# Kernel optimization log

Measured on AMD Instinct MI355X. Metric: run time of the kernel, lower is better.

Reference implementation:

```python
import jax, jax.numpy as jnp
import numpy as np

N_HEADS = 16
D_EMBED = 1024
D_HEAD = D_EMBED // N_HEADS  # 64
B, S = 2, 2048


def setup_inputs() -> dict:
    key = jax.random.key(0)
    ks = jax.random.split(key, 6)
    k = jax.random.normal(ks[0], (B, S, D_EMBED), dtype=jnp.float32)
    q = jax.random.normal(ks[1], (B, S, D_EMBED), dtype=jnp.float32)
    v = jax.random.normal(ks[2], (B, S, D_EMBED), dtype=jnp.float32)
    # per-head projections, shared across heads (nn.Linear(d_head, d_head, bias=False))
    scale = 1.0 / np.sqrt(D_HEAD)
    Wk = jax.random.normal(ks[3], (D_HEAD, D_HEAD), dtype=jnp.float32) * scale
    Wq = jax.random.normal(ks[4], (D_HEAD, D_HEAD), dtype=jnp.float32) * scale
    Wv = jax.random.normal(ks[5], (D_HEAD, D_HEAD), dtype=jnp.float32) * scale
    return {"k": k, "q": q, "v": v, "Wk": Wk, "Wq": Wq, "Wv": Wv}


def reference(k, q, v, Wk, Wq, Wv):
    b, s, _ = k.shape
    # split heads: [b, s, h, dh]
    kh = k.reshape(b, s, N_HEADS, D_HEAD)
    qh = q.reshape(b, s, N_HEADS, D_HEAD)
    vh = v.reshape(b, s, N_HEADS, D_HEAD)
    # shared per-head linear projection (y = x @ W^T, torch Linear convention)
    kh = jnp.einsum('bshd,ed->bshe', kh, Wk)
    qh = jnp.einsum('bshd,ed->bshe', qh, Wq)
    vh = jnp.einsum('bshd,ed->bshe', vh, Wv)
    # attention scores [b, h, q, k]
    scores = jnp.einsum('bqhd,bkhd->bhqk', qh, kh) / np.sqrt(D_HEAD).astype(np.float32)
    attn = jax.nn.softmax(scores, axis=-1)
    out = jnp.einsum('bhqk,bkhd->bqhd', attn, vh)
    return out.reshape(b, s, D_EMBED)
```

## Files before the change

### kernel.cpp

```cpp
#include <hip/hip_runtime.h>
#include <hip/hip_bf16.h>

typedef unsigned short u16;
typedef __bf16 bf16x8 __attribute__((ext_vector_type(8)));
typedef float f32x4 __attribute__((ext_vector_type(4)));

#define S_LEN 2048
#define NH 16
#define NB 2
#define HEAD_ELEMS (NB * NH * S_LEN * 64)

#if __has_builtin(__builtin_amdgcn_exp2f)
#define EXP2(x) __builtin_amdgcn_exp2f(x)
#else
#define EXP2(x) exp2f(x)
#endif

#define QSCALE 0.180336880f
#define SHIFT2 30.0f

__device__ __forceinline__ bf16x8 pack8(float4 a, float4 b, float sc) {
    union { bf16x8 v; __hip_bfloat162 h[4]; } r;
    r.h[0] = __float22bfloat162_rn(make_float2(a.x * sc, a.y * sc));
    r.h[1] = __float22bfloat162_rn(make_float2(a.z * sc, a.w * sc));
    r.h[2] = __float22bfloat162_rn(make_float2(b.x * sc, b.y * sc));
    r.h[3] = __float22bfloat162_rn(make_float2(b.z * sc, b.w * sc));
    return r.v;
}

__global__ __launch_bounds__(256) void proj_mfma(
    const float* __restrict__ kin, const float* __restrict__ qin, const float* __restrict__ vin,
    const float* __restrict__ Wk, const float* __restrict__ Wq, const float* __restrict__ Wv,
    u16* __restrict__ Kh, u16* __restrict__ Qh, u16* __restrict__ Vt)
{
    const int tid = threadIdx.x;
    const int wave = tid >> 6;
    const int lane = tid & 63;
    const int quad = lane >> 4;
    const int l15 = lane & 15;
    const int wid = blockIdx.x * 4 + wave;
    const int stile = wid >> 3;
    const int hg = wid & 7;
    const long row0 = (long)stile * 16;
    const int b = (int)(row0 >> 11);
    const int s0 = (int)(row0 & 2047);

    bf16x8 wf[3][4][2];
    const float* Ws[3] = {Wk, Wq, Wv};
    #pragma unroll
    for (int p = 0; p < 3; ++p) {
        const float sc = (p == 1) ? QSCALE : 1.0f;
        #pragma unroll
        for (int t = 0; t < 4; ++t) {
            const float* wr = Ws[p] + (t * 16 + l15) * 64 + quad * 8;
            wf[p][t][0] = pack8(*(const float4*)(wr),      *(const float4*)(wr + 4),  sc);
            wf[p][t][1] = pack8(*(const float4*)(wr + 32), *(const float4*)(wr + 36), sc);
        }
    }

    const float* xs[3] = {kin, qin, vin};

    #pragma unroll
    for (int hp = 0; hp < 2; ++hp) {
        const int h = hg * 2 + hp;
        const int bh = b * NH + h;
        bf16x8 xf[3][2];
        #pragma unroll
        for (int p = 0; p < 3; ++p) {
            const float* xr = xs[p] + (row0 + l15) * 1024 + h * 64 + quad * 8;
            xf[p][0] = pack8(*(const float4*)(xr),      *(const float4*)(xr + 4),  1.0f);
            xf[p][1] = pack8(*(const float4*)(xr + 32), *(const float4*)(xr + 36), 1.0f);
        }

        #pragma unroll
        for (int p = 0; p < 2; ++p) {
            u16* dst = (p == 0 ? Kh : Qh) + (long)bh * S_LEN * 64;
            #pragma unroll
            for (int nt = 0; nt < 4; ++nt) {
                f32x4 c = (f32x4){0.f, 0.f, 0.f, 0.f};
                c = __builtin_amdgcn_mfma_f32_16x16x32_bf16(xf[p][0], wf[p][nt][0], c, 0, 0, 0);
                c = __builtin_amdgcn_mfma_f32_16x16x32_bf16(xf[p][1], wf[p][nt][1], c, 0, 0, 0);
                #pragma unroll
                for (int r = 0; r < 4; ++r) {
                    union { __hip_bfloat162 h; u16 u[2]; } t2;
                    t2.h = __float22bfloat162_rn(make_float2(c[r], 0.f));
                    dst[((long)(s0 + quad * 4 + r)) * 64 + nt * 16 + l15] = t2.u[0];
                }
            }
        }

        {
            u16* dst = Vt + (long)bh * 64 * S_LEN;
            #pragma unroll
            for (int dt = 0; dt < 4; ++dt) {
                f32x4 c = (f32x4){0.f, 0.f, 0.f, 0.f};
                c = __builtin_amdgcn_mfma_f32_16x16x32_bf16(wf[2][dt][0], xf[2][0], c, 0, 0, 0);
                c = __builtin_amdgcn_mfma_f32_16x16x32_bf16(wf[2][dt][1], xf[2][1], c, 0, 0, 0);
                #pragma unroll
                for (int r = 0; r < 4; ++r) {
                    union { __hip_bfloat162 h; u16 u[2]; } t2;
                    t2.h = __float22bfloat162_rn(make_float2(c[r], 0.f));
                    dst[((long)(dt * 16 + quad * 4 + r)) * S_LEN + s0 + l15] = t2.u[0];
                }
            }
        }
    }
}

__global__ __launch_bounds__(256, 2) void attn_kernel(
    const u16* __restrict__ Qh, const u16* __restrict__ Kh,
    const u16* __restrict__ Vt, float* __restrict__ out)
{
    __shared__ __align__(16) u16 Pld[4][16 * 72];
    __shared__ __align__(16) float Old[4][64 * 40];
    __shared__ float lbc[4][64];

    const int tid = threadIdx.x;
    const int wave = tid >> 6;
    const int lane = tid & 63;
    const int quad = lane >> 4;
    const int l15 = lane & 15;
    const int qb = blockIdx.x;
    const int bh = blockIdx.y;
    const int b = bh >> 4, h = bh & 15;
    const int q0 = qb * 64;
    const u16* kb = Kh + (long)bh * S_LEN * 64;
    const u16* vb = Vt + (long)bh * 64 * S_LEN;

    bf16x8 qf[4][2];
    {
        const u16* qp = Qh + (long)bh * S_LEN * 64;
        #pragma unroll
        for (int g = 0; g < 4; ++g) {
            const u16* qr = qp + (long)(q0 + g * 16 + l15) * 64 + quad * 8;
            qf[g][0] = *(const bf16x8*)(qr);
            qf[g][1] = *(const bf16x8*)(qr + 32);
        }
    }

    const int rot = 16 * (l15 & 3);
    u16* pbase = &Pld[wave][l15 * 72];
    const int pwc[4] = {( 0 + quad * 4 + rot) & 63, (16 + quad * 4 + rot) & 63,
                        (32 + quad * 4 + rot) & 63, (48 + quad * 4 + rot) & 63};
    const int prc[2] = {(quad * 8 + rot) & 63, (32 + quad * 8 + rot) & 63};

    f32x4 oacc[4][4];
    #pragma unroll
    for (int g = 0; g < 4; ++g)
        #pragma unroll
        for (int dt = 0; dt < 4; ++dt) oacc[g][dt] = (f32x4){0.f, 0.f, 0.f, 0.f};
    float rs[4] = {0.f, 0.f, 0.f, 0.f};

    for (int kt = wave; kt < S_LEN / 64; kt += 4) {
        const u16* kt_p = kb + (long)kt * 64 * 64;
        const u16* vt_p = vb + kt * 64;
        bf16x8 kf[4][2], vf[4][2];
        #pragma unroll
        for (int n = 0; n < 4; ++n) {
            const u16* kr = kt_p + (n * 16 + l15) * 64 + quad * 8;
            kf[n][0] = *(const bf16x8*)(kr);
            kf[n][1] = *(const bf16x8*)(kr + 32);
        }
        #pragma unroll
        for (int dt = 0; dt < 4; ++dt) {
            const u16* vr = vt_p + (long)(dt * 16 + l15) * S_LEN + quad * 8;
            vf[dt][0] = *(const bf16x8*)(vr);
            vf[dt][1] = *(const bf16x8*)(vr + 32);
        }

        #pragma unroll
        for (int g = 0; g < 4; ++g) {
            f32x4 sacc[4];
            #pragma unroll
            for (int n = 0; n < 4; ++n) {
                f32x4 c = (f32x4){0.f, 0.f, 0.f, 0.f};
                c = __builtin_amdgcn_mfma_f32_16x16x32_bf16(kf[n][0], qf[g][0], c, 0, 0, 0);
                c = __builtin_amdgcn_mfma_f32_16x16x32_bf16(kf[n][1], qf[g][1], c, 0, 0, 0);
                sacc[n] = c;
            }
            #pragma unroll
            for (int n = 0; n < 4; ++n) {
                float p0 = EXP2(sacc[n][0] - SHIFT2);
                float p1 = EXP2(sacc[n][1] - SHIFT2);
                float p2 = EXP2(sacc[n][2] - SHIFT2);
                float p3 = EXP2(sacc[n][3] - SHIFT2);
                rs[g] += (p0 + p1) + (p2 + p3);
                union { uint2 w; __hip_bfloat162 h[2]; } pk;
                pk.h[0] = __float22bfloat162_rn(make_float2(p0, p1));
                pk.h[1] = __float22bfloat162_rn(make_float2(p2, p3));
                *(uint2*)(pbase + pwc[n]) = pk.w;
            }
            bf16x8 pf0 = *(const bf16x8*)(pbase + prc[0]);
            bf16x8 pf1 = *(const bf16x8*)(pbase + prc[1]);
            #pragma unroll
            for (int dt = 0; dt < 4; ++dt) {
                f32x4 o = oacc[g][dt];
                o = __builtin_amdgcn_mfma_f32_16x16x32_bf16(vf[dt][0], pf0, o, 0, 0, 0);
                o = __builtin_amdgcn_mfma_f32_16x16x32_bf16(vf[dt][1], pf1, o, 0, 0, 0);
                oacc[g][dt] = o;
            }
        }
    }

    #pragma unroll
    for (int g = 0; g < 4; ++g) {
        rs[g] += __shfl_xor(rs[g], 16);
        rs[g] += __shfl_xor(rs[g], 32);
    }
    if (lane < 16) {
        #pragma unroll
        for (int g = 0; g < 4; ++g) lbc[wave][g * 16 + lane] = rs[g];
    }

    const int rq = tid >> 2, seg = tid & 3;
    #pragma unroll
    for (int half = 0; half < 2; ++half) {
        #pragma unroll
        for (int g = 0; g < 4; ++g)
            #pragma unroll
            for (int d2 = 0; d2 < 2; ++d2)
                *(f32x4*)&Old[wave][(g * 16 + l15) * 40 + d2 * 16 + quad * 4] = oacc[g][half * 2 + d2];
        __syncthreads();
        f32x4 a0 = (f32x4){0.f, 0.f, 0.f, 0.f}, a1 = a0;
        #pragma unroll
        for (int w = 0; w < 4; ++w) {
            a0 += *(const f32x4*)&Old[w][rq * 40 + seg * 8];
            a1 += *(const f32x4*)&Old[w][rq * 40 + seg * 8 + 4];
        }
        const float linv = 1.0f / (lbc[0][rq] + lbc[1][rq] + lbc[2][rq] + lbc[3][rq]);
        float* op = out + ((long)(b * S_LEN + q0 + rq)) * 1024 + h * 64 + half * 32 + seg * 8;
        float4 s0 = make_float4(a0[0] * linv, a0[1] * linv, a0[2] * linv, a0[3] * linv);
        float4 s1 = make_float4(a1[0] * linv, a1[1] * linv, a1[2] * linv, a1[3] * linv);
        *(float4*)(op) = s0;
        *(float4*)(op + 4) = s1;
        __syncthreads();
    }
}

extern "C" void kernel_launch(void* const* d_in, const int* in_sizes, int n_in,
                              void* d_out, int out_size, void* d_ws, size_t ws_size,
                              hipStream_t stream) {
    const float* kin = (const float*)d_in[0];
    const float* qin = (const float*)d_in[1];
    const float* vin = (const float*)d_in[2];
    const float* Wk  = (const float*)d_in[3];
    const float* Wq  = (const float*)d_in[4];
    const float* Wv  = (const float*)d_in[5];
    float* out = (float*)d_out;

    u16* wsp = (u16*)d_ws;
    u16* Kh = wsp;
    u16* Qh = wsp + (long)HEAD_ELEMS;
    u16* Vt = wsp + 2 * (long)HEAD_ELEMS;

    proj_mfma<<<512, 256, 0, stream>>>(kin, qin, vin, Wk, Wq, Wv, Kh, Qh, Vt);
    dim3 g(S_LEN / 64, NB * NH);
    attn_kernel<<<g, 256, 0, stream>>>(Qh, Kh, Vt, out);
}
```

Measured before the change: 177.7 us.

## Split projection into K/Q and V kernels with LDS-staged coalesced stores; prefetch K in attention

Splits the combined projection kernel into separate K/Q and V kernels. Each stages its bf16 results in shared memory and then writes them to global memory with 16-byte coalesced stores, replacing the scattered 2-byte stores. The attention kernel now prefetches the next K tile into registers, uses launch_bounds occupancy 3, and shrinks the output reduction buffer to four phases of 16 columns. This adds one more kernel launch and extra register pressure from the prefetch buffers.

After: 374.7 us. +110.9%, slower.

```diff
diff --git a/kernel.cpp b/kernel.cpp
--- a/kernel.cpp
+++ b/kernel.cpp
@@ -28,91 +28,131 @@
     return r.v;
 }
 
-__global__ __launch_bounds__(256) void proj_mfma(
-    const float* __restrict__ kin, const float* __restrict__ qin, const float* __restrict__ vin,
-    const float* __restrict__ Wk, const float* __restrict__ Wq, const float* __restrict__ Wv,
-    u16* __restrict__ Kh, u16* __restrict__ Qh, u16* __restrict__ Vt)
+__global__ __launch_bounds__(256) void proj_kq(
+    const float* __restrict__ kin, const float* __restrict__ qin,
+    const float* __restrict__ Wk, const float* __restrict__ Wq,
+    u16* __restrict__ Kh, u16* __restrict__ Qh)
 {
+    __shared__ __align__(16) u16 Yld[8 * 16 * 72];
+
     const int tid = threadIdx.x;
     const int wave = tid >> 6;
     const int lane = tid & 63;
     const int quad = lane >> 4;
     const int l15 = lane & 15;
-    const int wid = blockIdx.x * 4 + wave;
-    const int stile = wid >> 3;
-    const int hg = wid & 7;
+    const int stile = blockIdx.x;
+    const int p = blockIdx.y;
+    const int hh = blockIdx.z;
     const long row0 = (long)stile * 16;
     const int b = (int)(row0 >> 11);
     const int s0 = (int)(row0 & 2047);
 
-    bf16x8 wf[3][4][2];
-    const float* Ws[3] = {Wk, Wq, Wv};
-    #pragma unroll
-    for (int p = 0; p < 3; ++p) {
-        const float sc = (p == 1) ? QSCALE : 1.0f;
-        #pragma unroll
-        for (int t = 0; t < 4; ++t) {
-            const float* wr = Ws[p] + (t * 16 + l15) * 64 + quad * 8;
-            wf[p][t][0] = pack8(*(const float4*)(wr),      *(const float4*)(wr + 4),  sc);
-            wf[p][t][1] = pack8(*(const float4*)(wr + 32), *(const float4*)(wr + 36), sc);
-        }
-    }
-
-    const float* xs[3] = {kin, qin, vin};
+    const float* X = p ? qin : kin;
+    const float* W = p ? Wq : Wk;
+    const float sc = p ? QSCALE : 1.0f;
+
+    bf16x8 wf[4][2];
+    #pragma unroll
+    for (int nt = 0; nt < 4; ++nt) {
+        const float* wr = W + (nt * 16 + l15) * 64 + quad * 8;
+        wf[nt][0] = pack8(*(const float4*)(wr),      *(const float4*)(wr + 4),  sc);
+        wf[nt][1] = pack8(*(const float4*)(wr + 32), *(const float4*)(wr + 36), sc);
+    }
 
     #pragma unroll
     for (int hp = 0; hp < 2; ++hp) {
-        const int h = hg * 2 + hp;
-        const int bh = b * NH + h;
-        bf16x8 xf[3][2];
-        #pragma unroll
-        for (int p = 0; p < 3; ++p) {
-            const float* xr = xs[p] + (row0 + l15) * 1024 + h * 64 + quad * 8;
-            xf[p][0] = pack8(*(const float4*)(xr),      *(const float4*)(xr + 4),  1.0f);
-            xf[p][1] = pack8(*(const float4*)(xr + 32), *(const float4*)(xr + 36), 1.0f);
-        }
-
-        #pragma unroll
-        for (int p = 0; p < 2; ++p) {
-            u16* dst = (p == 0 ? Kh : Qh) + (long)bh * S_LEN * 64;
-            #pragma unroll
-            for (int nt = 0; nt < 4; ++nt) {
-                f32x4 c = (f32x4){0.f, 0.f, 0.f, 0.f};
-                c = __builtin_amdgcn_mfma_f32_16x16x32_bf16(xf[p][0], wf[p][nt][0], c, 0, 0, 0);
-                c = __builtin_amdgcn_mfma_f32_16x16x32_bf16(xf[p][1], wf[p][nt][1], c, 0, 0, 0);
-                #pragma unroll
-                for (int r = 0; r < 4; ++r) {
-                    union { __hip_bfloat162 h; u16 u[2]; } t2;
-                    t2.h = __float22bfloat162_rn(make_float2(c[r], 0.f));
-                    dst[((long)(s0 + quad * 4 + r)) * 64 + nt * 16 + l15] = t2.u[0];
-                }
-            }
-        }
-
-        {
-            u16* dst = Vt + (long)bh * 64 * S_LEN;
-            #pragma unroll
-            for (int dt = 0; dt < 4; ++dt) {
-                f32x4 c = (f32x4){0.f, 0.f, 0.f, 0.f};
-                c = __builtin_amdgcn_mfma_f32_16x16x32_bf16(wf[2][dt][0], xf[2][0], c, 0, 0, 0);
-                c = __builtin_amdgcn_mfma_f32_16x16x32_bf16(wf[2][dt][1], xf[2][1], c, 0, 0, 0);
-                #pragma unroll
-                for (int r = 0; r < 4; ++r) {
-                    union { __hip_bfloat162 h; u16 u[2]; } t2;
-                    t2.h = __float22bfloat162_rn(make_float2(c[r], 0.f));
-                    dst[((long)(dt * 16 + quad * 4 + r)) * S_LEN + s0 + l15] = t2.u[0];
-                }
-            }
-        }
-    }
-}
-
-__global__ __launch_bounds__(256, 2) void attn_kernel(
+        const int hl = wave * 2 + hp;
+        const int h = hh * 8 + hl;
+        const float* xr = X + (row0 + l15) * 1024 + h * 64 + quad * 8;
+        bf16x8 a0 = pack8(*(const float4*)(xr),      *(const float4*)(xr + 4),  1.0f);
+        bf16x8 a1 = pack8(*(const float4*)(xr + 32), *(const float4*)(xr + 36), 1.0f);
+        #pragma unroll
+        for (int nt = 0; nt < 4; ++nt) {
+            f32x4 c = (f32x4){0.f, 0.f, 0.f, 0.f};
+            c = __builtin_amdgcn_mfma_f32_16x16x32_bf16(a0, wf[nt][0], c, 0, 0, 0);
+            c = __builtin_amdgcn_mfma_f32_16x16x32_bf16(a1, wf[nt][1], c, 0, 0, 0);
+            union { __hip_bfloat162 h2; u16 u[2]; } x01, x23;
+            x01.h2 = __float22bfloat162_rn(make_float2(c[0], c[1]));
+            x23.h2 = __float22bfloat162_rn(make_float2(c[2], c[3]));
+            int base = (hl * 16 + quad * 4) * 72 + nt * 16 + l15;
+            Yld[base]       = x01.u[0];
+            Yld[base + 72]  = x01.u[1];
+            Yld[base + 144] = x23.u[0];
+            Yld[base + 216] = x23.u[1];
+        }
+    }
+    __syncthreads();
+
+    u16* dst = p ? Qh : Kh;
+    #pragma unroll
+    for (int it = 0; it < 4; ++it) {
+        int idx = tid + it * 256;
+        int eg = idx & 7, s = (idx >> 3) & 15, hl = idx >> 7;
+        int bh = b * NH + hh * 8 + hl;
+        *(float4*)(dst + ((long)bh * S_LEN + s0 + s) * 64 + eg * 8) =
+            *(const float4*)&Yld[(hl * 16 + s) * 72 + eg * 8];
+    }
+}
+
+__global__ __launch_bounds__(256) void proj_v(
+    const float* __restrict__ vin, const float* __restrict__ Wv, u16* __restrict__ Vt)
+{
+    __shared__ __align__(16) u16 Vtile[64 * 72];
+
+    const int tid = threadIdx.x;
+    const int wave = tid >> 6;
+    const int lane = tid & 63;
+    const int quad = lane >> 4;
+    const int l15 = lane & 15;
+    const long row0 = (long)blockIdx.x * 64;
+    const int b = (int)(row0 >> 11);
+    const int s0 = (int)(row0 & 2047);
+    const int h = blockIdx.y;
+    const int bh = b * NH + h;
+
+    bf16x8 wf[4][2];
+    #pragma unroll
+    for (int dt = 0; dt < 4; ++dt) {
+        const float* wr = Wv + (dt * 16 + l15) * 64 + quad * 8;
+        wf[dt][0] = pack8(*(const float4*)(wr),      *(const float4*)(wr + 4),  1.0f);
+        wf[dt][1] = pack8(*(const float4*)(wr + 32), *(const float4*)(wr + 36), 1.0f);
+    }
+
+    const float* xr = vin + (row0 + wave * 16 + l15) * 1024 + h * 64 + quad * 8;
+    bf16x8 x0 = pack8(*(const float4*)(xr),      *(const float4*)(xr + 4),  1.0f);
+    bf16x8 x1 = pack8(*(const float4*)(xr + 32), *(const float4*)(xr + 36), 1.0f);
+
+    #pragma unroll
+    for (int dt = 0; dt < 4; ++dt) {
+        f32x4 c = (f32x4){0.f, 0.f, 0.f, 0.f};
+        c = __builtin_amdgcn_mfma_f32_16x16x32_bf16(wf[dt][0], x0, c, 0, 0, 0);
+        c = __builtin_amdgcn_mfma_f32_16x16x32_bf16(wf[dt][1], x1, c, 0, 0, 0);
+        int base = (dt * 16 + quad * 4) * 72 + wave * 16 + l15;
+        union { __hip_bfloat162 h2; u16 u[2]; } x01, x23;
+        x01.h2 = __float22bfloat162_rn(make_float2(c[0], c[1]));
+        x23.h2 = __float22bfloat162_rn(make_float2(c[2], c[3]));
+        Vtile[base]       = x01.u[0];
+        Vtile[base + 72]  = x01.u[1];
+        Vtile[base + 144] = x23.u[0];
+        Vtile[base + 216] = x23.u[1];
+    }
+    __syncthreads();
+
+    u16* dst = Vt + (long)bh * 64 * S_LEN + s0;
+    #pragma unroll
+    for (int it = 0; it < 2; ++it) {
+        int idx = tid + it * 256;
+        int sg = idx & 7, e = idx >> 3;
+        *(float4*)(dst + (long)e * S_LEN + sg * 8) = *(const float4*)&Vtile[e * 72 + sg * 8];
+    }
+}
+
+__global__ __launch_bounds__(256, 3) void attn_kernel(
     const u16* __restrict__ Qh, const u16* __restrict__ Kh,
     const u16* __restrict__ Vt, float* __restrict__ out)
 {
     __shared__ __align__(16) u16 Pld[4][16 * 72];
-    __shared__ __align__(16) float Old[4][64 * 40];
+    __shared__ __align__(16) float Old[4][64 * 20];
     __shared__ float lbc[4][64];
 
     const int tid = threadIdx.x;
@@ -151,21 +191,34 @@
         for (int dt = 0; dt < 4; ++dt) oacc[g][dt] = (f32x4){0.f, 0.f, 0.f, 0.f};
     float rs[4] = {0.f, 0.f, 0.f, 0.f};
 
-    for (int kt = wave; kt < S_LEN / 64; kt += 4) {
-        const u16* kt_p = kb + (long)kt * 64 * 64;
-        const u16* vt_p = vb + kt * 64;
-        bf16x8 kf[4][2], vf[4][2];
+    bf16x8 kf[4][2], knx[4][2];
+    {
+        const u16* kt_p = kb + (long)wave * 64 * 64;
         #pragma unroll
         for (int n = 0; n < 4; ++n) {
             const u16* kr = kt_p + (n * 16 + l15) * 64 + quad * 8;
             kf[n][0] = *(const bf16x8*)(kr);
             kf[n][1] = *(const bf16x8*)(kr + 32);
         }
+    }
+
+    for (int kt = wave; kt < S_LEN / 64; kt += 4) {
+        bf16x8 vf[4][2];
+        const u16* vt_p = vb + kt * 64;
         #pragma unroll
         for (int dt = 0; dt < 4; ++dt) {
             const u16* vr = vt_p + (long)(dt * 16 + l15) * S_LEN + quad * 8;
             vf[dt][0] = *(const bf16x8*)(vr);
             vf[dt][1] = *(const bf16x8*)(vr + 32);
+        }
+        if (kt + 4 < S_LEN / 64) {
+            const u16* kp = kb + (long)(kt + 4) * 64 * 64;
+            #pragma unroll
+            for (int n = 0; n < 4; ++n) {
+                const u16* kr = kp + (n * 16 + l15) * 64 + quad * 8;
+                knx[n][0] = *(const bf16x8*)(kr);
+                knx[n][1] = *(const bf16x8*)(kr + 32);
+            }
         }
 
         #pragma unroll
@@ -185,9 +238,9 @@
                 float p2 = EXP2(sacc[n][2] - SHIFT2);
                 float p3 = EXP2(sacc[n][3] - SHIFT2);
                 rs[g] += (p0 + p1) + (p2 + p3);
-                union { uint2 w; __hip_bfloat162 h[2]; } pk;
-                pk.h[0] = __float22bfloat162_rn(make_float2(p0, p1));
-                pk.h[1] = __float22bfloat162_rn(make_float2(p2, p3));
+                union { uint2 w; __hip_bfloat162 h2[2]; } pk;
+                pk.h2[0] = __float22bfloat162_rn(make_float2(p0, p1));
+                pk.h2[1] = __float22bfloat162_rn(make_float2(p2, p3));
                 *(uint2*)(pbase + pwc[n]) = pk.w;
             }
             bf16x8 pf0 = *(const bf16x8*)(pbase + prc[0]);
@@ -200,6 +253,11 @@
                 oacc[g][dt] = o;
             }
         }
+        #pragma unroll
+        for (int n = 0; n < 4; ++n) {
+            kf[n][0] = knx[n][0];
+            kf[n][1] = knx[n][1];
+        }
     }
 
     #pragma unroll
@@ -211,28 +269,23 @@
         #pragma unroll
         for (int g = 0; g < 4; ++g) lbc[wave][g * 16 + lane] = rs[g];
     }
+    __syncthreads();
 
     const int rq = tid >> 2, seg = tid & 3;
-    #pragma unroll
-    for (int half = 0; half < 2; ++half) {
+    const float linv = 1.0f / (lbc[0][rq] + lbc[1][rq] + lbc[2][rq] + lbc[3][rq]);
+    float* op = out + ((long)(b * S_LEN + q0 + rq)) * 1024 + h * 64;
+
+    #pragma unroll
+    for (int ph = 0; ph < 4; ++ph) {
         #pragma unroll
         for (int g = 0; g < 4; ++g)
-            #pragma unroll
-            for (int d2 = 0; d2 < 2; ++d2)
-                *(f32x4*)&Old[wave][(g * 16 + l15) * 40 + d2 * 16 + quad * 4] = oacc[g][half * 2 + d2];
+            *(f32x4*)&Old[wave][(g * 16 + l15) * 20 + quad * 4] = oacc[g][ph];
         __syncthreads();
-        f32x4 a0 = (f32x4){0.f, 0.f, 0.f, 0.f}, a1 = a0;
-        #pragma unroll
-        for (int w = 0; w < 4; ++w) {
-            a0 += *(const f32x4*)&Old[w][rq * 40 + seg * 8];
-            a1 += *(const f32x4*)&Old[w][rq * 40 + seg * 8 + 4];
-        }
-        const float linv = 1.0f / (lbc[0][rq] + lbc[1][rq] + lbc[2][rq] + lbc[3][rq]);
-        float* op = out + ((long)(b * S_LEN + q0 + rq)) * 1024 + h * 64 + half * 32 + seg * 8;
-        float4 s0 = make_float4(a0[0] * linv, a0[1] * linv, a0[2] * linv, a0[3] * linv);
-        float4 s1 = make_float4(a1[0] * linv, a1[1] * linv, a1[2] * linv, a1[3] * linv);
-        *(float4*)(op) = s0;
-        *(float4*)(op + 4) = s1;
+        f32x4 a = (f32x4){0.f, 0.f, 0.f, 0.f};
+        #pragma unroll
+        for (int w = 0; w < 4; ++w) a += *(const f32x4*)&Old[w][rq * 20 + seg * 4];
+        *(float4*)(op + ph * 16 + seg * 4) =
+            make_float4(a[0] * linv, a[1] * linv, a[2] * linv, a[3] * linv);
         __syncthreads();
     }
 }
@@ -253,7 +306,10 @@
     u16* Qh = wsp + (long)HEAD_ELEMS;
     u16* Vt = wsp + 2 * (long)HEAD_ELEMS;
 
-    proj_mfma<<<512, 256, 0, stream>>>(kin, qin, vin, Wk, Wq, Wv, Kh, Qh, Vt);
+    dim3 kqg(256, 2, 2);
+    proj_kq<<<kqg, 256, 0, stream>>>(kin, qin, Wk, Wq, Kh, Qh);
+    dim3 vg(64, 16);
+    proj_v<<<vg, 256, 0, stream>>>(vin, Wv, Vt);
     dim3 g(S_LEN / 64, NB * NH);
     attn_kernel<<<g, 256, 0, stream>>>(Qh, Kh, Vt, out);
 }
```
